# Kernel optimization log

Measured on AMD Instinct MI355X. Metric: run time of the kernel, lower is better.

## Reference

```python
import jax, jax.numpy as jnp
import numpy as np

N = 50000      # nodes
E = 800000     # edges (before self-loops)
F = 128        # num_features
H = 64         # hidden_channels
B = 512        # batch_size (num graphs)
NC = 10        # num_classes


def setup_inputs() -> dict:
    key = jax.random.key(0)
    ks = jax.random.split(key, 24)
    rn = lambda k, shp, s=0.05: jax.random.normal(k, shp, jnp.float32) * s
    inp = {}
    inp["x"] = jax.random.normal(ks[0], (N, F), jnp.float32)
    inp["edge_index"] = jax.random.randint(ks[1], (2, E), 0, N)
    inp["batch"] = jnp.sort(jax.random.randint(ks[2], (N,), 0, B))
    # GATConv1: in F -> 4 heads x H (concat)
    inp["W1"] = rn(ks[3], (F, 4 * H)); inp["a_src1"] = rn(ks[4], (4, H))
    inp["a_dst1"] = rn(ks[5], (4, H)); inp["b1"] = rn(ks[6], (4 * H,))
    # GATConv2: in 4H -> 1 head x 2H
    inp["W2"] = rn(ks[7], (4 * H, 2 * H)); inp["a_src2"] = rn(ks[8], (1, 2 * H))
    inp["a_dst2"] = rn(ks[9], (1, 2 * H)); inp["b2"] = rn(ks[10], (2 * H,))
    # GCNConv: in 2H -> H
    inp["Wg"] = rn(ks[11], (2 * H, H)); inp["bg"] = rn(ks[12], (H,))
    # BatchNorms (eval mode: running_mean=0, running_var=1)
    inp["bn1_g"] = 1.0 + rn(ks[13], (4 * H,)); inp["bn1_b"] = rn(ks[14], (4 * H,))
    inp["bn2_g"] = 1.0 + rn(ks[15], (2 * H,)); inp["bn2_b"] = rn(ks[16], (2 * H,))
    inp["bn3_g"] = 1.0 + rn(ks[17], (2 * H,)); inp["bn3_b"] = rn(ks[18], (2 * H,))
    inp["lin1_W"] = rn(ks[19], (H, 128)); inp["lin1_b"] = rn(ks[20], (128,))
    inp["lin2_W"] = rn(ks[21], (128, NC)); inp["lin2_b"] = rn(ks[22], (NC,))
    inp["batch_size"] = B
    return inp


def _gat(x, src, dst, W, a_s, a_d, b, n):
    """PyG GATConv (eval): project, edge attention (leaky_relu 0.2), dst-softmax, scatter."""
    heads, ch = a_s.shape
    h = (x @ W).reshape(n, heads, ch)                       # [N, heads, ch]
    sc_s = (h * a_s).sum(-1)                                # [N, heads]
    sc_d = (h * a_d).sum(-1)
    e = jax.nn.leaky_relu(sc_s[src] + sc_d[dst], 0.2)       # [E2, heads]
    m = jax.ops.segment_max(e, dst, num_segments=n)
    ee = jnp.exp(e - m[dst])
    s = jax.ops.segment_sum(ee, dst, num_segments=n)
    alpha = ee / (s[dst] + 1e-16)                           # edge softmax per dst
    out = jax.ops.segment_sum(h[src] * alpha[:, :, None], dst, num_segments=n)
    return out.reshape(n, heads * ch) + b


def _bn_eval(x, g, b, eps=1e-5):
    # BatchNorm1d eval with running_mean=0, running_var=1
    return x * (g / jnp.sqrt(1.0 + eps)) + b


def reference(x, edge_index, batch, W1, a_src1, a_dst1, b1, W2, a_src2, a_dst2, b2,
              Wg, bg, bn1_g, bn1_b, bn2_g, bn2_b, bn3_g, bn3_b,
              lin1_W, lin1_b, lin2_W, lin2_b, batch_size):
    n = x.shape[0]
    loop = jnp.arange(n)
    src = jnp.concatenate([edge_index[0], loop])            # add self-loops (PyG default)
    dst = jnp.concatenate([edge_index[1], loop])
    lrelu = lambda v: jax.nn.leaky_relu(v, 0.01)            # module's LeakyReLU()

    x1 = _bn_eval(lrelu(_gat(x, src, dst, W1, a_src1, a_dst1, b1, n)), bn1_g, bn1_b)
    x2 = _bn_eval(lrelu(_gat(x1, src, dst, W2, a_src2, a_dst2, b2, n)), bn2_g, bn2_b)

    # GCNConv with symmetric normalization over A + I
    deg = jax.ops.segment_sum(jnp.ones_like(dst, jnp.float32), dst, num_segments=n)
    dis = jnp.where(deg > 0, jax.lax.rsqrt(deg), 0.0)
    h = x2 @ Wg                                             # [N, H]
    msg = h[src] * (dis[src] * dis[dst])[:, None]
    x3 = lrelu(jax.ops.segment_sum(msg, dst, num_segments=n) + bg)

    # global_mean_pool over graphs (dropout is identity in eval)
    sums = jax.ops.segment_sum(x3, batch, num_segments=batch_size)
    cnt = jax.ops.segment_sum(jnp.ones((n,), jnp.float32), batch, num_segments=batch_size)
    pooled = sums / jnp.clip(cnt, 1.0)[:, None]             # [B, H]

    y = lrelu(_bn_eval(pooled @ lin1_W + lin1_b, bn3_g, bn3_b))
    return y @ lin2_W + lin2_b                              # [B, NC]
```

## Files before the change

### kernel.cpp

```cpp
#include <hip/hip_runtime.h>
#include <hip/hip_bf16.h>

#define NN  50000
#define EE  800000
#define NE2 850000
#define NB  512
#define NRT 3125
#define NSB 196
#define NEB ((NE2 + 255) / 256)

#define BN_RS 0.9999950000374997f

typedef __attribute__((ext_vector_type(8))) short short8;
typedef __attribute__((ext_vector_type(4))) float f32x4;

__device__ __forceinline__ float bf2f(__hip_bfloat16 v) { return __bfloat162float(v); }
__device__ __forceinline__ unsigned short f2b(float v) {
    __hip_bfloat16 b = __float2bfloat16(v);
    return *reinterpret_cast<unsigned short*>(&b);
}
__device__ __forceinline__ float u2f(unsigned short u) {
    union { unsigned u; float f; } c; c.u = ((unsigned)u) << 16; return c.f;
}
__device__ __forceinline__ float lrelu01(float v) { return v > 0.f ? v : 0.01f * v; }
__device__ __forceinline__ float lrelu02(float v) { return v > 0.f ? v : 0.2f * v; }

__device__ __forceinline__ void up2(unsigned u, float& lo, float& hi) {
    union { unsigned x; float f; } a, b;
    a.x = u << 16; b.x = u & 0xFFFF0000u;
    lo = a.f; hi = b.f;
}
__device__ __forceinline__ void acc8(float* acc, uint4 u, float e) {
    float lo, hi;
    up2(u.x, lo, hi); acc[0] = fmaf(lo, e, acc[0]); acc[1] = fmaf(hi, e, acc[1]);
    up2(u.y, lo, hi); acc[2] = fmaf(lo, e, acc[2]); acc[3] = fmaf(hi, e, acc[3]);
    up2(u.z, lo, hi); acc[4] = fmaf(lo, e, acc[4]); acc[5] = fmaf(hi, e, acc[5]);
    up2(u.w, lo, hi); acc[6] = fmaf(lo, e, acc[6]); acc[7] = fmaf(hi, e, acc[7]);
}
__device__ __forceinline__ unsigned packbf2(float lo, float hi) {
    return ((unsigned)f2b(hi) << 16) | (unsigned)f2b(lo);
}

__device__ __forceinline__ void edge_sd(const int* __restrict__ ei, int e, int& s, int& d) {
    if (e < EE) { s = ei[e]; d = ei[EE + e]; }
    else        { s = e - EE; d = e - EE; }
}

__device__ __forceinline__ float ldf(const void* p, int i, bool bf) {
    return bf ? bf2f(((const __hip_bfloat16*)p)[i]) : ((const float*)p)[i];
}

#define NSEG 20
#define WTOT 85578
#define XQUADS (NN * 32)
#define PREP_TOT (NE2 + XQUADS + WTOT + 32768 + 32768 + 8192)
struct SegArgs { const void* src[NSEG]; int off[NSEG]; };

__global__ __launch_bounds__(256) void prep_k(SegArgs a,
                                              const void* __restrict__ x_raw,
                                              ushort4* __restrict__ xb4,
                                              const void* __restrict__ W1r,
                                              const void* __restrict__ W2r,
                                              const void* __restrict__ Wgr,
                                              float* __restrict__ wf,
                                              unsigned short* __restrict__ W1t,
                                              unsigned short* __restrict__ W2t,
                                              unsigned short* __restrict__ Wgt,
                                              const int* __restrict__ ei,
                                              int* __restrict__ degi,
                                              int* __restrict__ rank,
                                              int* __restrict__ flag) {
    __shared__ int cnt;
    int t = threadIdx.x;
    if (t == 0) cnt = 0;
    __syncthreads();
    {
        int c = 0;
        const unsigned* xw = (const unsigned*)x_raw;
#pragma unroll
        for (int k = 0; k < 4; ++k) {
            unsigned w = xw[t * 4 + k];
            unsigned ef = (w >> 7) & 0xFFu;
            if (ef >= 100u && ef <= 140u) c++;
        }
        atomicAdd(&cnt, c);
    }
    __syncthreads();
    bool bf = (cnt > 512);
    if (blockIdx.x == 0 && t == 0) *flag = bf ? 1 : 0;

    int i = blockIdx.x * 256 + t;
    if (i >= PREP_TOT) return;
    if (i < NE2) {
        int s, d; edge_sd(ei, i, s, d);
        rank[i] = atomicAdd(&degi[d], 1);
        return;
    }
    i -= NE2;
    if (i < XQUADS) {
        ushort4 o;
        if (bf) o = ((const ushort4*)x_raw)[i];
        else {
            float4 v = ((const float4*)x_raw)[i];
            o.x = f2b(v.x); o.y = f2b(v.y); o.z = f2b(v.z); o.w = f2b(v.w);
        }
        xb4[i] = o;
        return;
    }
    i -= XQUADS;
    if (i < WTOT) {
        int s = 0;
#pragma unroll
        for (int k = 1; k < NSEG; ++k) if (i >= a.off[k]) s = k;
        wf[i] = ldf(a.src[s], i - a.off[s], bf);
        return;
    }
    i -= WTOT;
    if (i < 32768) {
        int n = i >> 7, k = i & 127;
        W1t[i] = f2b(ldf(W1r, k * 256 + n, bf));
        return;
    }
    i -= 32768;
    if (i < 32768) {
        int n = i >> 8, k = i & 255;
        W2t[i] = f2b(ldf(W2r, k * 128 + n, bf));
        return;
    }
    i -= 32768;
    {
        int n = i >> 7, k = i & 127;
        Wgt[i] = f2b(ldf(Wgr, k * 64 + n, bf));
    }
}

__global__ __launch_bounds__(256) void pscan_k(const int* __restrict__ degi,
                                               int* __restrict__ incl, int* __restrict__ bsum) {
    __shared__ int tmp[256];
    int t = threadIdx.x;
    int i = blockIdx.x * 256 + t;
    int v = (i < NN) ? degi[i] : 0;
    tmp[t] = v;
    __syncthreads();
#pragma unroll
    for (int off = 1; off < 256; off <<= 1) {
        int u = (t >= off) ? tmp[t - off] : 0;
        __syncthreads();
        tmp[t] += u;
        __syncthreads();
    }
    if (i < NN) incl[i] = tmp[t];
    if (t == 255) bsum[blockIdx.x] = tmp[255];
}

__global__ __launch_bounds__(256) void bscan_k(int* __restrict__ bsum) {
    __shared__ int tmp[256];
    int t = threadIdx.x;
    tmp[t] = (t < NSB) ? bsum[t] : 0;
    __syncthreads();
#pragma unroll
    for (int off = 1; off < 256; off <<= 1) {
        int u = (t >= off) ? tmp[t - off] : 0;
        __syncthreads();
        tmp[t] += u;
        __syncthreads();
    }
    if (t < NSB) bsum[t] = tmp[t];
}

__global__ __launch_bounds__(256) void fscan_k(const int* __restrict__ degi,
                                               const int* __restrict__ incl,
                                               const int* __restrict__ bsum,
                                               const int* __restrict__ batch,
                                               int* __restrict__ row_ptr,
                                               float* __restrict__ dis, int* __restrict__ gstart) {
    int i = blockIdx.x * 256 + threadIdx.x;
    if (i <= NB) {
        int lo = 0, hi = NN;
        while (lo < hi) { int mid = (lo + hi) >> 1; if (batch[mid] < i) lo = mid + 1; else hi = mid; }
        gstart[i] = lo;
    }
    if (i >= NN) return;
    int dg = degi[i];
    int base = (blockIdx.x > 0) ? bsum[blockIdx.x - 1] : 0;
    int ex = base + incl[i] - dg;
    row_ptr[i] = ex;
    dis[i] = dg > 0 ? rsqrtf((float)dg) : 0.f;
    if (i == NN - 1) row_ptr[NN] = bsum[NSB - 1];
}

__global__ __launch_bounds__(256) void scatter_k(const int* __restrict__ ei,
                                                 const int* __restrict__ row_ptr,
                                                 const int* __restrict__ rank,
                                                 int* __restrict__ csr_src) {
    int e = blockIdx.x * 256 + threadIdx.x;
    if (e >= NE2) return;
    int s, d; edge_sd(ei, e, s, d);
    csr_src[row_ptr[d] + rank[e]] = s;
}

__global__ __launch_bounds__(256) void mgemm1_k(const short* __restrict__ A,
                                                const short* __restrict__ Bt,
                                                unsigned short* __restrict__ C,
                                                const float* __restrict__ a_s,
                                                const float* __restrict__ a_d,
                                                float* __restrict__ sc_s,
                                                float* __restrict__ sc_d) {
    int wave = threadIdx.x >> 6, lane = threadIdx.x & 63;
    int cg = wave;
    int l15 = lane & 15, quad = lane >> 4;
    const short* bp = Bt + (size_t)(cg * 64 + l15) * 128 + quad * 8;
    short8 bfr[4][4];
#pragma unroll
    for (int j = 0; j < 4; ++j)
#pragma unroll
        for (int kk = 0; kk < 4; ++kk)
            bfr[j][kk] = *(const short8*)(bp + (size_t)j * 16 * 128 + kk * 32);
    float asv[4], adv[4];
#pragma unroll
    for (int j = 0; j < 4; ++j) {
        asv[j] = a_s[cg * 64 + j * 16 + l15];
        adv[j] = a_d[cg * 64 + j * 16 + l15];
    }
#pragma unroll
    for (int rtl = 0; rtl < 4; ++rtl) {
        int rt = blockIdx.x * 4 + rtl;
        if (rt >= NRT) break;
        const short* ap = A + (size_t)(rt * 16 + l15) * 128 + quad * 8;
        f32x4 acc[4] = {};
#pragma unroll
        for (int kk = 0; kk < 4; ++kk) {
            short8 a = *(const short8*)(ap + kk * 32);
#pragma unroll
            for (int j = 0; j < 4; ++j)
                acc[j] = __builtin_amdgcn_mfma_f32_16x16x32_bf16(a, bfr[j][kk], acc[j], 0, 0, 0);
        }
        float ss[4] = {0.f, 0.f, 0.f, 0.f}, sd[4] = {0.f, 0.f, 0.f, 0.f};
#pragma unroll
        for (int j = 0; j < 4; ++j) {
            int n = cg * 64 + j * 16 + l15;
#pragma unroll
            for (int r = 0; r < 4; ++r) {
                float v = acc[j][r];
                C[(size_t)(rt * 16 + quad * 4 + r) * 256 + n] = f2b(v);
                ss[r] = fmaf(v, asv[j], ss[r]);
                sd[r] = fmaf(v, adv[j], sd[r]);
            }
        }
#pragma unroll
        for (int off = 1; off < 16; off <<= 1) {
#pragma unroll
            for (int r = 0; r < 4; ++r) {
                ss[r] += __shfl_xor(ss[r], off);
                sd[r] += __shfl_xor(sd[r], off);
            }
        }
        if (l15 == 0) {
#pragma unroll
            for (int r = 0; r < 4; ++r) {
                int node = rt * 16 + quad * 4 + r;
                sc_s[node * 4 + cg] = ss[r];
                sc_d[node * 4 + cg] = sd[r];
            }
        }
    }
}

__global__ __launch_bounds__(256) void mgemm2_k(const short* __restrict__ A,
                                                const short* __restrict__ Bt,
                                                unsigned short* __restrict__ C,
                                                const float* __restrict__ a_s,
                                                const float* __restrict__ a_d,
                                                float* __restrict__ sc_s,
                                                float* __restrict__ sc_d) {
    __shared__ float sred[4][16][2];
    int wave = threadIdx.x >> 6, lane = threadIdx.x & 63;
    int gidx = blockIdx.x * 4 + wave;
    bool act = gidx < NRT * 2;
    int gcl = act ? gidx : NRT * 2 - 1;
    int rt = gcl >> 1, cg = gcl & 1;
    int l15 = lane & 15, quad = lane >> 4;
    const short* ap = A + (size_t)(rt * 16 + l15) * 256 + quad * 8;
    const short* bp = Bt + (size_t)(cg * 64 + l15) * 256 + quad * 8;
    f32x4 acc[4] = {};
    for (int k0 = 0; k0 < 256; k0 += 32) {
        short8 a = *(const short8*)(ap + k0);
#pragma unroll
        for (int j = 0; j < 4; ++j) {
            short8 b = *(const short8*)(bp + (size_t)j * 16 * 256 + k0);
            acc[j] = __builtin_amdgcn_mfma_f32_16x16x32_bf16(a, b, acc[j], 0, 0, 0);
        }
    }
    float asv[4], adv[4];
#pragma unroll
    for (int j = 0; j < 4; ++j) {
        asv[j] = a_s[cg * 64 + j * 16 + l15];
        adv[j] = a_d[cg * 64 + j * 16 + l15];
    }
    float ss[4] = {0.f, 0.f, 0.f, 0.f}, sd[4] = {0.f, 0.f, 0.f, 0.f};
#pragma unroll
    for (int j = 0; j < 4; ++j) {
        int n = cg * 64 + j * 16 + l15;
#pragma unroll
        for (int r = 0; r < 4; ++r) {
            float v = acc[j][r];
            if (act) C[(size_t)(rt * 16 + quad * 4 + r) * 128 + n] = f2b(v);
            ss[r] = fmaf(v, asv[j], ss[r]);
            sd[r] = fmaf(v, adv[j], sd[r]);
        }
    }
#pragma unroll
    for (int off = 1; off < 16; off <<= 1) {
#pragma unroll
        for (int r = 0; r < 4; ++r) {
            ss[r] += __shfl_xor(ss[r], off);
            sd[r] += __shfl_xor(sd[r], off);
        }
    }
    if (l15 == 0) {
#pragma unroll
        for (int r = 0; r < 4; ++r) {
            sred[wave][quad * 4 + r][0] = ss[r];
            sred[wave][quad * 4 + r][1] = sd[r];
        }
    }
    __syncthreads();
    if (threadIdx.x < 32) {
        int rl = threadIdx.x >> 4, row = threadIdx.x & 15;
        int g2 = blockIdx.x * 4 + rl * 2;
        if (g2 < NRT * 2) {
            int node = (g2 >> 1) * 16 + row;
            sc_s[node] = sred[rl * 2][row][0] + sred[rl * 2 + 1][row][0];
            sc_d[node] = sred[rl * 2][row][1] + sred[rl * 2 + 1][row][1];
        }
    }
}

__global__ __launch_bounds__(256) void mgemm3_k(const short* __restrict__ A,
                                                const short* __restrict__ Bt,
                                                unsigned short* __restrict__ C) {
    int wave = threadIdx.x >> 6, lane = threadIdx.x & 63;
    int wt = blockIdx.x * 4 + wave;
    int l15 = lane & 15, quad = lane >> 4;
    const short* bp = Bt + (size_t)l15 * 128 + quad * 8;
    short8 bfr[4][4];
#pragma unroll
    for (int j = 0; j < 4; ++j)
#pragma unroll
        for (int kk = 0; kk < 4; ++kk)
            bfr[j][kk] = *(const short8*)(bp + (size_t)j * 16 * 128 + kk * 32);
#pragma unroll
    for (int rtl = 0; rtl < 4; ++rtl) {
        int rt = wt * 4 + rtl;
        if (rt >= NRT) break;
        const short* ap = A + (size_t)(rt * 16 + l15) * 128 + quad * 8;
        f32x4 acc[4] = {};
#pragma unroll
        for (int kk = 0; kk < 4; ++kk) {
            short8 a = *(const short8*)(ap + kk * 32);
#pragma unroll
            for (int j = 0; j < 4; ++j)
                acc[j] = __builtin_amdgcn_mfma_f32_16x16x32_bf16(a, bfr[j][kk], acc[j], 0, 0, 0);
        }
#pragma unroll
        for (int j = 0; j < 4; ++j) {
            int n = j * 16 + l15;
#pragma unroll
            for (int r = 0; r < 4; ++r)
                C[(size_t)(rt * 16 + quad * 4 + r) * 64 + n] = f2b(acc[j][r]);
        }
    }
}

__device__ __forceinline__ float sel4(float4 v, int head) {
    float ab = (head & 1) ? v.y : v.x;
    float cd = (head & 1) ? v.w : v.z;
    return (head & 2) ? cd : ab;
}

__global__ __launch_bounds__(256) void agg1_k(const int* __restrict__ row_ptr,
                                              const int* __restrict__ csr_src,
                                              const uint4* __restrict__ h1b,
                                              const float* __restrict__ sc_s,
                                              const float4* __restrict__ sc_d4,
                                              const float4* __restrict__ b1,
                                              const float4* __restrict__ g1,
                                              const float4* __restrict__ bb1,
                                              uint4* __restrict__ x1b) {
    int n = __builtin_amdgcn_readfirstlane((blockIdx.x * 256 + threadIdx.x) >> 6);
    int lane = threadIdx.x & 63;
    if (n >= NN) return;
    int g = lane >> 5, sl = lane & 31;
    int head = sl >> 3;
    int row = row_ptr[n], end = row_ptr[n + 1];
    float scd_h = sel4(sc_d4[n], head);
    float acc[8] = {0.f, 0.f, 0.f, 0.f, 0.f, 0.f, 0.f, 0.f};
    float den = 0.f;
    int c = row;
    for (; c + 7 < end; c += 8) {
        int i0 = c + g, i1 = c + 2 + g, i2 = c + 4 + g, i3 = c + 6 + g;
        int s0 = csr_src[i0], s1 = csr_src[i1], s2 = csr_src[i2], s3 = csr_src[i3];
        float w0 = sc_s[s0 * 4 + head], w1 = sc_s[s1 * 4 + head];
        float w2 = sc_s[s2 * 4 + head], w3 = sc_s[s3 * 4 + head];
        uint4 u0 = h1b[(size_t)s0 * 32 + sl];
        uint4 u1 = h1b[(size_t)s1 * 32 + sl];
        uint4 u2 = h1b[(size_t)s2 * 32 + sl];
        uint4 u3 = h1b[(size_t)s3 * 32 + sl];
        float e0 = __expf(lrelu02(w0 + scd_h));
        float e1 = __expf(lrelu02(w1 + scd_h));
        float e2 = __expf(lrelu02(w2 + scd_h));
        float e3 = __expf(lrelu02(w3 + scd_h));
        den += (e0 + e1) + (e2 + e3);
        acc8(acc, u0, e0); acc8(acc, u1, e1); acc8(acc, u2, e2); acc8(acc, u3, e3);
    }
    if (c < end) {
        int i0 = c + g, i1 = c + 2 + g, i2 = c + 4 + g, i3 = c + 6 + g;
        bool v0 = i0 < end, v1 = i1 < end, v2 = i2 < end, v3 = i3 < end;
        int l = end - 1;
        int s0 = csr_src[v0 ? i0 : l], s1 = csr_src[v1 ? i1 : l];
        int s2 = csr_src[v2 ? i2 : l], s3 = csr_src[v3 ? i3 : l];
        float w0 = sc_s[s0 * 4 + head], w1 = sc_s[s1 * 4 + head];
        float w2 = sc_s[s2 * 4 + head], w3 = sc_s[s3 * 4 + head];
        uint4 u0 = h1b[(size_t)s0 * 32 + sl];
        uint4 u1 = h1b[(size_t)s1 * 32 + sl];
        uint4 u2 = h1b[(size_t)s2 * 32 + sl];
        uint4 u3 = h1b[(size_t)s3 * 32 + sl];
        float e0 = v0 ? __expf(lrelu02(w0 + scd_h)) : 0.f;
        float e1 = v1 ? __expf(lrelu02(w1 + scd_h)) : 0.f;
        float e2 = v2 ? __expf(lrelu02(w2 + scd_h)) : 0.f;
        float e3 = v3 ? __expf(lrelu02(w3 + scd_h)) : 0.f;
        den += (e0 + e1) + (e2 + e3);
        acc8(acc, u0, e0); acc8(acc, u1, e1); acc8(acc, u2, e2); acc8(acc, u3, e3);
    }
    den += __shfl_xor(den, 32);
#pragma unroll
    for (int k = 0; k < 8; ++k) acc[k] += __shfl_xor(acc[k], 32);
    if (g == 0) {
        float inv = 1.f / (den + 1e-16f);
        float4 bA = b1[sl * 2],  bB = b1[sl * 2 + 1];
        float4 gA = g1[sl * 2],  gB = g1[sl * 2 + 1];
        float4 eA = bb1[sl * 2], eB = bb1[sl * 2 + 1];
        float o0 = lrelu01(fmaf(acc[0], inv, bA.x)) * (gA.x * BN_RS) + eA.x;
        float o1 = lrelu01(fmaf(acc[1], inv, bA.y)) * (gA.y * BN_RS) + eA.y;
        float o2 = lrelu01(fmaf(acc[2], inv, bA.z)) * (gA.z * BN_RS) + eA.z;
        float o3 = lrelu01(fmaf(acc[3], inv, bA.w)) * (gA.w * BN_RS) + eA.w;
        float o4 = lrelu01(fmaf(acc[4], inv, bB.x)) * (gB.x * BN_RS) + eB.x;
        float o5 = lrelu01(fmaf(acc[5], inv, bB.y)) * (gB.y * BN_RS) + eB.y;
        float o6 = lrelu01(fmaf(acc[6], inv, bB.z)) * (gB.z * BN_RS) + eB.z;
        float o7 = lrelu01(fmaf(acc[7], inv, bB.w)) * (gB.w * BN_RS) + eB.w;
        uint4 w;
        w.x = packbf2(o0, o1); w.y = packbf2(o2, o3);
        w.z = packbf2(o4, o5); w.w = packbf2(o6, o7);
        x1b[(size_t)n * 32 + sl] = w;
    }
}

__global__ __launch_bounds__(256) void agg2_k(const int* __restrict__ row_ptr,
                                              const int* __restrict__ csr_src,
                                              const uint4* __restrict__ h2b,
                                              const float* __restrict__ sc_s,
                                              const float* __restrict__ sc_d,
                                              const float4* __restrict__ b2,
                                              const float4* __restrict__ g2,
                                              const float4* __restrict__ bb2,
                                              uint4* __restrict__ x2b) {
    int n = __builtin_amdgcn_readfirstlane((blockIdx.x * 256 + threadIdx.x) >> 6);
    int lane = threadIdx.x & 63;
    if (n >= NN) return;
    int g = lane >> 4, sl = lane & 15;
    int row = row_ptr[n], end = row_ptr[n + 1];
    float scd = sc_d[n];
    float acc[8] = {0.f, 0.f, 0.f, 0.f, 0.f, 0.f, 0.f, 0.f};
    float den = 0.f;
    int c = row;
    for (; c + 15 < end; c += 16) {
        int i0 = c + g, i1 = c + 4 + g, i2 = c + 8 + g, i3 = c + 12 + g;
        int s0 = csr_src[i0], s1 = csr_src[i1], s2 = csr_src[i2], s3 = csr_src[i3];
        float c0 = sc_s[s0], c1 = sc_s[s1], c2 = sc_s[s2], c3 = sc_s[s3];
        uint4 u0 = h2b[(size_t)s0 * 16 + sl];
        uint4 u1 = h2b[(size_t)s1 * 16 + sl];
        uint4 u2 = h2b[(size_t)s2 * 16 + sl];
        uint4 u3 = h2b[(size_t)s3 * 16 + sl];
        float e0 = __expf(lrelu02(c0 + scd));
        float e1 = __expf(lrelu02(c1 + scd));
        float e2 = __expf(lrelu02(c2 + scd));
        float e3 = __expf(lrelu02(c3 + scd));
        den += (e0 + e1) + (e2 + e3);
        acc8(acc, u0, e0); acc8(acc, u1, e1); acc8(acc, u2, e2); acc8(acc, u3, e3);
    }
    if (c < end) {
        int i0 = c + g, i1 = c + 4 + g, i2 = c + 8 + g, i3 = c + 12 + g;
        bool v0 = i0 < end, v1 = i1 < end, v2 = i2 < end, v3 = i3 < end;
        int l = end - 1;
        int s0 = csr_src[v0 ? i0 : l], s1 = csr_src[v1 ? i1 : l];
        int s2 = csr_src[v2 ? i2 : l], s3 = csr_src[v3 ? i3 : l];
        float c0 = sc_s[s0], c1 = sc_s[s1], c2 = sc_s[s2], c3 = sc_s[s3];
        uint4 u0 = h2b[(size_t)s0 * 16 + sl];
        uint4 u1 = h2b[(size_t)s1 * 16 + sl];
        uint4 u2 = h2b[(size_t)s2 * 16 + sl];
        uint4 u3 = h2b[(size_t)s3 * 16 + sl];
        float e0 = v0 ? __expf(lrelu02(c0 + scd)) : 0.f;
        float e1 = v1 ? __expf(lrelu02(c1 + scd)) : 0.f;
        float e2 = v2 ? __expf(lrelu02(c2 + scd)) : 0.f;
        float e3 = v3 ? __expf(lrelu02(c3 + scd)) : 0.f;
        den += (e0 + e1) + (e2 + e3);
        acc8(acc, u0, e0); acc8(acc, u1, e1); acc8(acc, u2, e2); acc8(acc, u3, e3);
    }
    den += __shfl_xor(den, 16);
    den += __shfl_xor(den, 32);
#pragma unroll
    for (int k = 0; k < 8; ++k) {
        acc[k] += __shfl_xor(acc[k], 16);
        acc[k] += __shfl_xor(acc[k], 32);
    }
    if (lane < 16) {
        float inv = 1.f / (den + 1e-16f);
        float4 bA = b2[sl * 2],  bB = b2[sl * 2 + 1];
        float4 gA = g2[sl * 2],  gB = g2[sl * 2 + 1];
        float4 eA = bb2[sl * 2], eB = bb2[sl * 2 + 1];
        float o0 = lrelu01(fmaf(acc[0], inv, bA.x)) * (gA.x * BN_RS) + eA.x;
        float o1 = lrelu01(fmaf(acc[1], inv, bA.y)) * (gA.y * BN_RS) + eA.y;
        float o2 = lrelu01(fmaf(acc[2], inv, bA.z)) * (gA.z * BN_RS) + eA.z;
        float o3 = lrelu01(fmaf(acc[3], inv, bA.w)) * (gA.w * BN_RS) + eA.w;
        float o4 = lrelu01(fmaf(acc[4], inv, bB.x)) * (gB.x * BN_RS) + eB.x;
        float o5 = lrelu01(fmaf(acc[5], inv, bB.y)) * (gB.y * BN_RS) + eB.y;
        float o6 = lrelu01(fmaf(acc[6], inv, bB.z)) * (gB.z * BN_RS) + eB.z;
        float o7 = lrelu01(fmaf(acc[7], inv, bB.w)) * (gB.w * BN_RS) + eB.w;
        uint4 w;
        w.x = packbf2(o0, o1); w.y = packbf2(o2, o3);
        w.z = packbf2(o4, o5); w.w = packbf2(o6, o7);
        x2b[(size_t)n * 16 + sl] = w;
    }
}

__global__ __launch_bounds__(256) void gcn_k(const int* __restrict__ row_ptr,
                                             const int* __restrict__ csr_src,
                                             const uint4* __restrict__ hgb,
                                             const float* __restrict__ dis,
                                             const float4* __restrict__ bg,
                                             uint4* __restrict__ x3b) {
    int n = __builtin_amdgcn_readfirstlane((blockIdx.x * 256 + threadIdx.x) >> 6);
    int lane = threadIdx.x & 63;
    if (n >= NN) return;
    int g = lane >> 3, sl = lane & 7;
    int row = row_ptr[n], end = row_ptr[n + 1];
    float dn = dis[n];
    float acc[8] = {0.f, 0.f, 0.f, 0.f, 0.f, 0.f, 0.f, 0.f};
    int c = row;
    for (; c + 15 < end; c += 16) {
        int i0 = c + g, i1 = c + 8 + g;
        int s0 = csr_src[i0], s1 = csr_src[i1];
        float w0 = dis[s0], w1 = dis[s1];
        uint4 u0 = hgb[(size_t)s0 * 8 + sl];
        uint4 u1 = hgb[(size_t)s1 * 8 + sl];
        acc8(acc, u0, w0); acc8(acc, u1, w1);
    }
    if (c < end) {
        int i0 = c + g, i1 = c + 8 + g;
        bool v0 = i0 < end, v1 = i1 < end;
        int l = end - 1;
        int s0 = csr_src[v0 ? i0 : l], s1 = csr_src[v1 ? i1 : l];
        float w0 = v0 ? dis[s0] : 0.f, w1 = v1 ? dis[s1] : 0.f;
        uint4 u0 = hgb[(size_t)s0 * 8 + sl];
        uint4 u1 = hgb[(size_t)s1 * 8 + sl];
        acc8(acc, u0, w0); acc8(acc, u1, w1);
    }
#pragma unroll
    for (int off = 8; off <= 32; off <<= 1) {
#pragma unroll
        for (int k = 0; k < 8; ++k) acc[k] += __shfl_xor(acc[k], off);
    }
    if (lane < 8) {
        float4 bA = bg[sl * 2], bB = bg[sl * 2 + 1];
        float o0 = lrelu01(fmaf(acc[0], dn, bA.x));
        float o1 = lrelu01(fmaf(acc[1], dn, bA.y));
        float o2 = lrelu01(fmaf(acc[2], dn, bA.z));
        float o3 = lrelu01(fmaf(acc[3], dn, bA.w));
        float o4 = lrelu01(fmaf(acc[4], dn, bB.x));
        float o5 = lrelu01(fmaf(acc[5], dn, bB.y));
        float o6 = lrelu01(fmaf(acc[6], dn, bB.z));
        float o7 = lrelu01(fmaf(acc[7], dn, bB.w));
        uint4 w;
        w.x = packbf2(o0, o1); w.y = packbf2(o2, o3);
        w.z = packbf2(o4, o5); w.w = packbf2(o6, o7);
        x3b[(size_t)n * 8 + sl] = w;
    }
}

__global__ __launch_bounds__(256) void poolmlp_k(const unsigned short* __restrict__ x3b,
                                                 const int* __restrict__ gstart,
                                                 const float* __restrict__ l1W,
                                                 const float* __restrict__ l1b,
                                                 const float* __restrict__ g3,
                                                 const float* __restrict__ b3,
                                                 const float* __restrict__ l2W,
                                                 const float* __restrict__ l2b,
                                                 void* __restrict__ outp,
                                                 const int* __restrict__ flag) {
    __shared__ float red[4][64];
    __shared__ float pl[64];
    __shared__ float y1s[128];
    int g = blockIdx.x, t = threadIdx.x;
    int c = t & 63, r = t >> 6;
    int s = gstart[g], e = gstart[g + 1];
    float sum = 0.f;
    for (int n = s + r; n < e; n += 4) sum += u2f(x3b[(size_t)n * 64 + c]);
    red[r][c] = sum;
    __syncthreads();
    if (t < 64) {
        float v = red[0][t] + red[1][t] + red[2][t] + red[3][t];
        int cnt = e - s; if (cnt < 1) cnt = 1;
        pl[t] = v / (float)cnt;
    }
    __syncthreads();
    if (t < 128) {
        float acc = l1b[t];
#pragma unroll 8
        for (int j = 0; j < 64; ++j) acc = fmaf(pl[j], l1W[j * 128 + t], acc);
        acc = acc * (g3[t] * BN_RS) + b3[t];
        y1s[t] = lrelu01(acc);
    }
    __syncthreads();
    if (t < 10) {
        float o = l2b[t];
#pragma unroll 8
        for (int j = 0; j < 128; ++j) o = fmaf(y1s[j], l2W[j * 10 + t], o);
        if (*flag) ((__hip_bfloat16*)outp)[g * 10 + t] = __float2bfloat16(o);
        else       ((float*)outp)[g * 10 + t] = o;
    }
}

static const int kSegN[NSEG]  = {32768, 256, 256, 256, 32768, 128, 128, 128, 8192, 64,
                                 256, 256, 128, 128, 128, 128, 8192, 128, 1280, 10};
static const int kSegIn[NSEG] = {3, 4, 5, 6, 7, 8, 9, 10, 11, 12, 13, 14, 15, 16, 17, 18, 19, 20, 21, 22};

extern "C" void kernel_launch(void* const* d_in, const int* in_sizes, int n_in,
                              void* d_out, int out_size, void* d_ws, size_t ws_size,
                              hipStream_t stream) {
    const void* x_raw = d_in[0];
    const int*  ei    = (const int*)d_in[1];
    const int*  batch = (const int*)d_in[2];

    int*   flag = (int*)d_ws;
    float* ws   = (float*)d_ws;
    unsigned short* xb = (unsigned short*)(ws + 16);
    float* wf   = ws + 16 + (size_t)NN * 64;
    unsigned short* W1t = (unsigned short*)(wf + 85584);
    unsigned short* W2t = W1t + 32768;
    unsigned short* Wgt = W2t + 32768;
    unsigned short* h1b = Wgt + 8192;
    unsigned short* x1b = h1b + (size_t)NN * 256;
    unsigned short* x2b = x1b + (size_t)NN * 256;
    unsigned short* hgb = x2b + (size_t)NN * 128;
    unsigned short* x3b = hgb + (size_t)NN * 64;
    float* sc_s1 = (float*)(x3b + (size_t)NN * 64);
    float* sc_d1 = sc_s1 + (size_t)NN * 4;
    float* sc_s2 = sc_d1 + (size_t)NN * 4;
    float* sc_d2 = sc_s2 + NN;
    float* disb  = sc_d2 + NN;
    int*   gstart = (int*)(disb + NN);
    int*   degi   = gstart + NB + 4;
    int*   incl   = degi + NN;
    int*   bsum   = incl + NN;
    int*   row_ptr = bsum + 256;
    int*   csr_src = row_ptr + NN + 4;

    int*   rankb = (int*)x1b;

    int off[NSEG]; int o = 0;
    for (int s = 0; s < NSEG; ++s) { off[s] = o; o += kSegN[s]; }
    float* as1f = wf + off[1];  float* ad1f = wf + off[2];
    float* b1f  = wf + off[3];  float* as2f = wf + off[5];
    float* ad2f = wf + off[6];  float* b2f  = wf + off[7];
    float* bgf  = wf + off[9];  float* bn1g = wf + off[10]; float* bn1b = wf + off[11];
    float* bn2g = wf + off[12]; float* bn2b = wf + off[13]; float* bn3g = wf + off[14];
    float* bn3b = wf + off[15]; float* l1Wf = wf + off[16]; float* l1bf = wf + off[17];
    float* l2Wf = wf + off[18]; float* l2bf = wf + off[19];

    unsigned short* h2b = h1b;

    hipMemsetAsync(degi, 0, NN * sizeof(int), stream);
    SegArgs sa;
    for (int s = 0; s < NSEG; ++s) { sa.src[s] = d_in[kSegIn[s]]; sa.off[s] = off[s]; }
    prep_k<<<(PREP_TOT + 255) / 256, 256, 0, stream>>>(sa, x_raw, (ushort4*)xb,
                                                       d_in[3], d_in[7], d_in[11],
                                                       wf, W1t, W2t, Wgt, ei, degi, rankb, flag);

    pscan_k<<<NSB, 256, 0, stream>>>(degi, incl, bsum);
    bscan_k<<<1, 256, 0, stream>>>(bsum);
    fscan_k<<<NSB, 256, 0, stream>>>(degi, incl, bsum, batch, row_ptr, disb, gstart);
    scatter_k<<<NEB, 256, 0, stream>>>(ei, row_ptr, rankb, csr_src);

    mgemm1_k<<<(NRT + 3) / 4, 256, 0, stream>>>((const short*)xb, (const short*)W1t, h1b,
                                                as1f, ad1f, sc_s1, sc_d1);
    agg1_k<<<12500, 256, 0, stream>>>(row_ptr, csr_src, (const uint4*)h1b,
                                      sc_s1, (const float4*)sc_d1,
                                      (const float4*)b1f, (const float4*)bn1g,
                                      (const float4*)bn1b, (uint4*)x1b);

    mgemm2_k<<<(NRT * 2 + 3) / 4, 256, 0, stream>>>((const short*)x1b, (const short*)W2t, h2b,
                                                    as2f, ad2f, sc_s2, sc_d2);
    agg2_k<<<12500, 256, 0, stream>>>(row_ptr, csr_src, (const uint4*)h2b,
                                      sc_s2, sc_d2,
                                      (const float4*)b2f, (const float4*)bn2g,
                                      (const float4*)bn2b, (uint4*)x2b);

    mgemm3_k<<<(NRT + 15) / 16, 256, 0, stream>>>((const short*)x2b, (const short*)Wgt, hgb);
    gcn_k<<<12500, 256, 0, stream>>>(row_ptr, csr_src, (const uint4*)hgb, disb,
                                     (const float4*)bgf, (uint4*)x3b);
    poolmlp_k<<<NB, 256, 0, stream>>>(x3b, gstart, l1Wf, l1bf, bn3g, bn3b, l2Wf, l2bf,
                                      d_out, flag);
}
```

Measured before the change: 382.1 us.

## Fuse GCN projection into agg2 and fold block-sum scan into fscan

The second GAT aggregation kernel now keeps its normalized output row in shared memory and multiplies it directly by the GCN weight matrix with scalar FMAs, writing the projected rows. This removes the separate MFMA GEMM launch and the x2 intermediate round trip through memory. Separately, the single-block scan of block sums is removed, and each fscan block reduces the preceding block sums itself. The cost is 128 scalar FMAs per lane per node, with Wgt reads per wave, instead of the matrix-core path. The early return for out-of-range nodes was also dropped, which is safe because the grid matches NN exactly.

Measured after the change: 462.8 us. 1.21x slower.

```diff
diff --git a/kernel.cpp b/kernel.cpp
--- a/kernel.cpp
+++ b/kernel.cpp
@@ -153,28 +153,24 @@
     if (t == 255) bsum[blockIdx.x] = tmp[255];
 }
 
-__global__ __launch_bounds__(256) void bscan_k(int* __restrict__ bsum) {
-    __shared__ int tmp[256];
-    int t = threadIdx.x;
-    tmp[t] = (t < NSB) ? bsum[t] : 0;
-    __syncthreads();
-#pragma unroll
-    for (int off = 1; off < 256; off <<= 1) {
-        int u = (t >= off) ? tmp[t - off] : 0;
-        __syncthreads();
-        tmp[t] += u;
-        __syncthreads();
-    }
-    if (t < NSB) bsum[t] = tmp[t];
-}
-
 __global__ __launch_bounds__(256) void fscan_k(const int* __restrict__ degi,
                                                const int* __restrict__ incl,
                                                const int* __restrict__ bsum,
                                                const int* __restrict__ batch,
                                                int* __restrict__ row_ptr,
                                                float* __restrict__ dis, int* __restrict__ gstart) {
-    int i = blockIdx.x * 256 + threadIdx.x;
+    __shared__ int tmp[256];
+    int t = threadIdx.x, b = blockIdx.x;
+    int i = b * 256 + t;
+    int x = (t < NSB && t < b) ? bsum[t] : 0;
+    tmp[t] = x;
+    __syncthreads();
+#pragma unroll
+    for (int off = 128; off > 0; off >>= 1) {
+        if (t < off) tmp[t] += tmp[t + off];
+        __syncthreads();
+    }
+    int base = tmp[0];
     if (i <= NB) {
         int lo = 0, hi = NN;
         while (lo < hi) { int mid = (lo + hi) >> 1; if (batch[mid] < i) lo = mid + 1; else hi = mid; }
@@ -182,11 +178,10 @@
     }
     if (i >= NN) return;
     int dg = degi[i];
-    int base = (blockIdx.x > 0) ? bsum[blockIdx.x - 1] : 0;
     int ex = base + incl[i] - dg;
     row_ptr[i] = ex;
     dis[i] = dg > 0 ? rsqrtf((float)dg) : 0.f;
-    if (i == NN - 1) row_ptr[NN] = bsum[NSB - 1];
+    if (i == NN - 1) row_ptr[NN] = ex + dg;
 }
 
 __global__ __launch_bounds__(256) void scatter_k(const int* __restrict__ ei,
@@ -332,42 +327,6 @@
             int node = (g2 >> 1) * 16 + row;
             sc_s[node] = sred[rl * 2][row][0] + sred[rl * 2 + 1][row][0];
             sc_d[node] = sred[rl * 2][row][1] + sred[rl * 2 + 1][row][1];
-        }
-    }
-}
-
-__global__ __launch_bounds__(256) void mgemm3_k(const short* __restrict__ A,
-                                                const short* __restrict__ Bt,
-                                                unsigned short* __restrict__ C) {
-    int wave = threadIdx.x >> 6, lane = threadIdx.x & 63;
-    int wt = blockIdx.x * 4 + wave;
-    int l15 = lane & 15, quad = lane >> 4;
-    const short* bp = Bt + (size_t)l15 * 128 + quad * 8;
-    short8 bfr[4][4];
-#pragma unroll
-    for (int j = 0; j < 4; ++j)
-#pragma unroll
-        for (int kk = 0; kk < 4; ++kk)
-            bfr[j][kk] = *(const short8*)(bp + (size_t)j * 16 * 128 + kk * 32);
-#pragma unroll
-    for (int rtl = 0; rtl < 4; ++rtl) {
-        int rt = wt * 4 + rtl;
-        if (rt >= NRT) break;
-        const short* ap = A + (size_t)(rt * 16 + l15) * 128 + quad * 8;
-        f32x4 acc[4] = {};
-#pragma unroll
-        for (int kk = 0; kk < 4; ++kk) {
-            short8 a = *(const short8*)(ap + kk * 32);
-#pragma unroll
-            for (int j = 0; j < 4; ++j)
-                acc[j] = __builtin_amdgcn_mfma_f32_16x16x32_bf16(a, bfr[j][kk], acc[j], 0, 0, 0);
-        }
-#pragma unroll
-        for (int j = 0; j < 4; ++j) {
-            int n = j * 16 + l15;
-#pragma unroll
-            for (int r = 0; r < 4; ++r)
-                C[(size_t)(rt * 16 + quad * 4 + r) * 64 + n] = f2b(acc[j][r]);
         }
     }
 }
@@ -463,10 +422,12 @@
                                               const float4* __restrict__ b2,
                                               const float4* __restrict__ g2,
                                               const float4* __restrict__ bb2,
-                                              uint4* __restrict__ x2b) {
+                                              const uint4* __restrict__ Wgt4,
+                                              unsigned short* __restrict__ hgb) {
+    __shared__ float xsh[4][128];
+    int wave = threadIdx.x >> 6;
     int n = __builtin_amdgcn_readfirstlane((blockIdx.x * 256 + threadIdx.x) >> 6);
     int lane = threadIdx.x & 63;
-    if (n >= NN) return;
     int g = lane >> 4, sl = lane & 15;
     int row = row_ptr[n], end = row_ptr[n + 1];
     float scd = sc_d[n];
@@ -518,19 +479,29 @@
         float4 bA = b2[sl * 2],  bB = b2[sl * 2 + 1];
         float4 gA = g2[sl * 2],  gB = g2[sl * 2 + 1];
         float4 eA = bb2[sl * 2], eB = bb2[sl * 2 + 1];
-        float o0 = lrelu01(fmaf(acc[0], inv, bA.x)) * (gA.x * BN_RS) + eA.x;
-        float o1 = lrelu01(fmaf(acc[1], inv, bA.y)) * (gA.y * BN_RS) + eA.y;
-        float o2 = lrelu01(fmaf(acc[2], inv, bA.z)) * (gA.z * BN_RS) + eA.z;
-        float o3 = lrelu01(fmaf(acc[3], inv, bA.w)) * (gA.w * BN_RS) + eA.w;
-        float o4 = lrelu01(fmaf(acc[4], inv, bB.x)) * (gB.x * BN_RS) + eB.x;
-        float o5 = lrelu01(fmaf(acc[5], inv, bB.y)) * (gB.y * BN_RS) + eB.y;
-        float o6 = lrelu01(fmaf(acc[6], inv, bB.z)) * (gB.z * BN_RS) + eB.z;
-        float o7 = lrelu01(fmaf(acc[7], inv, bB.w)) * (gB.w * BN_RS) + eB.w;
-        uint4 w;
-        w.x = packbf2(o0, o1); w.y = packbf2(o2, o3);
-        w.z = packbf2(o4, o5); w.w = packbf2(o6, o7);
-        x2b[(size_t)n * 16 + sl] = w;
-    }
+        xsh[wave][sl * 8 + 0] = lrelu01(fmaf(acc[0], inv, bA.x)) * (gA.x * BN_RS) + eA.x;
+        xsh[wave][sl * 8 + 1] = lrelu01(fmaf(acc[1], inv, bA.y)) * (gA.y * BN_RS) + eA.y;
+        xsh[wave][sl * 8 + 2] = lrelu01(fmaf(acc[2], inv, bA.z)) * (gA.z * BN_RS) + eA.z;
+        xsh[wave][sl * 8 + 3] = lrelu01(fmaf(acc[3], inv, bA.w)) * (gA.w * BN_RS) + eA.w;
+        xsh[wave][sl * 8 + 4] = lrelu01(fmaf(acc[4], inv, bB.x)) * (gB.x * BN_RS) + eB.x;
+        xsh[wave][sl * 8 + 5] = lrelu01(fmaf(acc[5], inv, bB.y)) * (gB.y * BN_RS) + eB.y;
+        xsh[wave][sl * 8 + 6] = lrelu01(fmaf(acc[6], inv, bB.z)) * (gB.z * BN_RS) + eB.z;
+        xsh[wave][sl * 8 + 7] = lrelu01(fmaf(acc[7], inv, bB.w)) * (gB.w * BN_RS) + eB.w;
+    }
+    __syncthreads();
+    float hacc = 0.f;
+    const float* xr = xsh[wave];
+#pragma unroll
+    for (int kk = 0; kk < 16; ++kk) {
+        uint4 wv = Wgt4[lane * 16 + kk];
+        int kb = kk * 8;
+        float lo, hi;
+        up2(wv.x, lo, hi); hacc = fmaf(xr[kb + 0], lo, hacc); hacc = fmaf(xr[kb + 1], hi, hacc);
+        up2(wv.y, lo, hi); hacc = fmaf(xr[kb + 2], lo, hacc); hacc = fmaf(xr[kb + 3], hi, hacc);
+        up2(wv.z, lo, hi); hacc = fmaf(xr[kb + 4], lo, hacc); hacc = fmaf(xr[kb + 5], hi, hacc);
+        up2(wv.w, lo, hi); hacc = fmaf(xr[kb + 6], lo, hacc); hacc = fmaf(xr[kb + 7], hi, hacc);
+    }
+    hgb[(size_t)n * 64 + lane] = f2b(hacc);
 }
 
 __global__ __launch_bounds__(256) void gcn_k(const int* __restrict__ row_ptr,
@@ -650,8 +621,7 @@
     unsigned short* Wgt = W2t + 32768;
     unsigned short* h1b = Wgt + 8192;
     unsigned short* x1b = h1b + (size_t)NN * 256;
-    unsigned short* x2b = x1b + (size_t)NN * 256;
-    unsigned short* hgb = x2b + (size_t)NN * 128;
+    unsigned short* hgb = x1b + (size_t)NN * 256;
     unsigned short* x3b = hgb + (size_t)NN * 64;
     float* sc_s1 = (float*)(x3b + (size_t)NN * 64);
     float* sc_d1 = sc_s1 + (size_t)NN * 4;
@@ -687,7 +657,6 @@
                                                        wf, W1t, W2t, Wgt, ei, degi, rankb, flag);
 
     pscan_k<<<NSB, 256, 0, stream>>>(degi, incl, bsum);
-    bscan_k<<<1, 256, 0, stream>>>(bsum);
     fscan_k<<<NSB, 256, 0, stream>>>(degi, incl, bsum, batch, row_ptr, disb, gstart);
     scatter_k<<<NEB, 256, 0, stream>>>(ei, row_ptr, rankb, csr_src);
 
@@ -703,9 +672,8 @@
     agg2_k<<<12500, 256, 0, stream>>>(row_ptr, csr_src, (const uint4*)h2b,
                                       sc_s2, sc_d2,
                                       (const float4*)b2f, (const float4*)bn2g,
-                                      (const float4*)bn2b, (uint4*)x2b);
-
-    mgemm3_k<<<(NRT + 15) / 16, 256, 0, stream>>>((const short*)x2b, (const short*)Wgt, hgb);
+                                      (const float4*)bn2b, (const uint4*)Wgt, hgb);
+
     gcn_k<<<12500, 256, 0, stream>>>(row_ptr, csr_src, (const uint4*)hgb, disb,
                                      (const float4*)bgf, (uint4*)x3b);
     poolmlp_k<<<NB, 256, 0, stream>>>(x3b, gstart, l1Wf, l1bf, bn3g, bn3b, l2Wf, l2bf,
```
